# Kernel optimization log

Hardware: AMD Instinct MI355X
Metric: run time of the kernel (lower is better)

Reference implementation:

```python
import jax, jax.numpy as jnp
import numpy as np

BSZ, QLEN, KLEN = 2, 1024, 2048
QD = KD = VD = HID = 1024
NH = 16
HD = HID // NH
SCALE = 1.0 / (HD ** 0.5)
NEG_INF = -1e30


def setup_inputs() -> dict:
    key = jax.random.key(0)
    ks = jax.random.split(key, 8)
    query = jax.random.normal(ks[0], (BSZ, QLEN, QD), dtype=jnp.float32)
    k_in = jax.random.normal(ks[1], (BSZ, KLEN, KD), dtype=jnp.float32)
    v_in = jax.random.normal(ks[2], (BSZ, KLEN, VD), dtype=jnp.float32)
    attn_mask = jax.random.randint(ks[3], (BSZ, KLEN), 0, 2, dtype=jnp.int32)
    # xavier_uniform for Linear(in, out) without bias; stored as [in, out]
    def xavier(k, fan_in, fan_out):
        lim = (6.0 / (fan_in + fan_out)) ** 0.5
        return jax.random.uniform(k, (fan_in, fan_out), jnp.float32, -lim, lim)
    Wq = xavier(ks[4], QD, HID)
    Wk = xavier(ks[5], KD, HID)
    Wv = xavier(ks[6], VD, HID)
    Wo = xavier(ks[7], HID, QD)
    return {"query": query, "key": k_in, "value": v_in, "attn_mask": attn_mask,
            "Wq": Wq, "Wk": Wk, "Wv": Wv, "Wo": Wo}


def reference(query, key, value, attn_mask, Wq, Wk, Wv, Wo):
    bsz, qlen, _ = query.shape
    klen = key.shape[1]
    # projections -> [b, len, n_head, head_dim]
    head_q = (query @ Wq).reshape(bsz, qlen, NH, HD)
    head_k = (key @ Wk).reshape(bsz, klen, NH, HD)
    head_v = (value @ Wv).reshape(bsz, klen, NH, HD)
    # attn scores [b, i, j, n]
    attn_score = jnp.einsum('bind,bjnd->bijn', head_q, head_k) * SCALE
    # 2D mask [b, j]: broadcast over query dim (axis 1) and head dim (axis 3)
    mask = (attn_mask == 0)[:, None, :, None]
    attn_score = jnp.where(mask, NEG_INF, attn_score)
    # configurable activation: sigmoid (no normalization over klen)
    attn_prob = jax.nn.sigmoid(attn_score)
    attn_vec = jnp.einsum('bijn,bjnd->bind', attn_prob, head_v)
    attn_vec = attn_vec.reshape(bsz, qlen, HID)
    return attn_vec @ Wo
```

## Files before the change

### kernel.cpp

```cpp
#include <hip/hip_runtime.h>
#include <hip/hip_bf16.h>

#define BSZ 2
#define QLEN 1024
#define KLEN 2048
#define HID 1024
#define NH 16
#define HD 64
#define SCALE 0.125f

using f32x4 = __attribute__((ext_vector_type(4))) float;
using bf16x8 = __attribute__((ext_vector_type(8))) short;
using u32x4 = __attribute__((ext_vector_type(4))) unsigned int;
using u32x2 = __attribute__((ext_vector_type(2))) unsigned int;
typedef unsigned short u16;

__device__ __forceinline__ unsigned int cvtpk(float a, float b) {
    unsigned int r;
    asm("v_cvt_pk_bf16_f32 %0, %1, %2" : "=v"(r) : "v"(a), "v"(b));
    return r;
}
__device__ __forceinline__ unsigned int pack2bf(float a, float b) { return cvtpk(a, b); }
__device__ __forceinline__ u16 f2bf(float x) { return (u16)cvtpk(x, x); }
__device__ __forceinline__ f32x4 zero4() {
    f32x4 z = {0.0f, 0.0f, 0.0f, 0.0f};
    return z;
}

__device__ __forceinline__ void gl16(const void* g, void* l) {
    __builtin_amdgcn_global_load_lds(
        (const __attribute__((address_space(1))) void*)g,
        (__attribute__((address_space(3))) void*)l, 16, 0, 0);
}

template<int ROWS>
__device__ __forceinline__ void stage64(const u16* __restrict__ g, size_t gstride,
                                        u16* lds, int tid) {
    const int lane = tid & 63, wv = tid >> 6;
    constexpr int RPW = ROWS / 4;
#pragma unroll
    for (int c = 0; c < RPW / 8; ++c) {
        int row = wv * RPW + c * 8 + (lane >> 3);
        int cg = (lane & 7) ^ (row & 7);
        gl16(g + (size_t)row * gstride + cg * 8, lds + (size_t)(wv * RPW + c * 8) * 64);
    }
}

__global__ __launch_bounds__(256) void a2bf_kernel(
    const float* __restrict__ Aq, const float* __restrict__ Ak,
    const float* __restrict__ Av,
    u16* __restrict__ qbf, u16* __restrict__ kbf, u16* __restrict__ vbf)
{
    const int bid = blockIdx.x;
    const float* src; u16* dst; size_t base;
    if (bid < 1024)      { src = Aq; dst = qbf; base = (size_t)bid * 2048; }
    else if (bid < 3072) { src = Ak; dst = kbf; base = (size_t)(bid - 1024) * 2048; }
    else                 { src = Av; dst = vbf; base = (size_t)(bid - 3072) * 2048; }
    size_t e = base + (size_t)threadIdx.x * 8;
    float4 x0 = *(const float4*)&src[e];
    float4 x1 = *(const float4*)&src[e + 4];
    u32x4 w;
    w[0] = pack2bf(x0.x, x0.y); w[1] = pack2bf(x0.z, x0.w);
    w[2] = pack2bf(x1.x, x1.y); w[3] = pack2bf(x1.z, x1.w);
    *(u32x4*)&dst[e] = w;
}

__global__ __launch_bounds__(256) void wtrans_kernel(
    const float* __restrict__ W0, const float* __restrict__ W1,
    const float* __restrict__ W2, const float* __restrict__ W3,
    u16* __restrict__ T0, u16* __restrict__ T1,
    u16* __restrict__ T2, u16* __restrict__ T3)
{
    const float* W = blockIdx.z == 0 ? W0 : blockIdx.z == 1 ? W1 : blockIdx.z == 2 ? W2 : W3;
    u16* T = blockIdx.z == 0 ? T0 : blockIdx.z == 1 ? T1 : blockIdx.z == 2 ? T2 : T3;
    __shared__ float tile[64][65];
    const int tid = threadIdx.x;
    const int r0 = blockIdx.x * 64;
    const int c0 = blockIdx.y * 64;
#pragma unroll
    for (int i = 0; i < 4; ++i) {
        int ch = i * 256 + tid;
        int row = ch >> 4, cg = ch & 15;
        float4 x = *(const float4*)&W[(size_t)(r0 + row) * 1024 + c0 + cg * 4];
        tile[row][cg * 4 + 0] = x.x;
        tile[row][cg * 4 + 1] = x.y;
        tile[row][cg * 4 + 2] = x.z;
        tile[row][cg * 4 + 3] = x.w;
    }
    __syncthreads();
#pragma unroll
    for (int i = 0; i < 2; ++i) {
        int ch = i * 256 + tid;
        int orow = ch >> 3, ocg = ch & 7;
        u32x4 o;
#pragma unroll
        for (int j = 0; j < 4; ++j)
            o[j] = pack2bf(tile[ocg * 8 + 2 * j][orow], tile[ocg * 8 + 2 * j + 1][orow]);
        *(u32x4*)&T[(size_t)(c0 + orow) * 1024 + r0 + ocg * 8] = o;
    }
}

__global__ __launch_bounds__(256) void qkv_gemm_kernel(
    const u16* __restrict__ Aq, const u16* __restrict__ Ak, const u16* __restrict__ Av,
    const u16* __restrict__ Bq, const u16* __restrict__ Bk, const u16* __restrict__ Bv,
    u16* __restrict__ hq, u16* __restrict__ hk, u16* __restrict__ hvT)
{
    __shared__ u32x4 lds[2048];
    u16* As = (u16*)lds;
    u16* Bs = (u16*)(lds + 1024);

    const int i = blockIdx.x;
    const int bid = (i & 7) * 80 + (i >> 3);
    const u16* A; const u16* Bt; u16* C; int lb, task;
    if (bid < 128)      { task = 0; A = Aq; Bt = Bq; C = hq; lb = bid; }
    else if (bid < 384) { task = 1; A = Ak; Bt = Bk; C = hk; lb = bid - 128; }
    else                { task = 2; A = Av; Bt = Bv; C = nullptr; lb = bid - 384; }
    const int m0 = (lb >> 3) * 128, n0 = (lb & 7) * 128;

    const int tid = threadIdx.x;
    const int lane = tid & 63, wv = tid >> 6;
    const int wr = wv >> 1, wc = wv & 1;
    const int m = lane & 15, g = lane >> 4;

    f32x4 acc[4][4];
#pragma unroll
    for (int i2 = 0; i2 < 4; ++i2)
#pragma unroll
        for (int j = 0; j < 4; ++j) acc[i2][j] = zero4();

    for (int k0 = 0; k0 < 1024; k0 += 64) {
        stage64<128>(A  + (size_t)m0 * 1024 + k0, 1024, As, tid);
        stage64<128>(Bt + (size_t)n0 * 1024 + k0, 1024, Bs, tid);
        __syncthreads();
#pragma unroll
        for (int kk = 0; kk < 64; kk += 32) {
            bf16x8 af[4], bfr[4];
#pragma unroll
            for (int mi = 0; mi < 4; ++mi) {
                int row = wr * 64 + mi * 16 + m;
                af[mi] = *(const bf16x8*)&As[(row * 64 + kk + g * 8) ^ ((row & 7) << 3)];
            }
#pragma unroll
            for (int ni = 0; ni < 4; ++ni) {
                int row = wc * 64 + ni * 16 + m;
                bfr[ni] = *(const bf16x8*)&Bs[(row * 64 + kk + g * 8) ^ ((row & 7) << 3)];
            }
#pragma unroll
            for (int mi = 0; mi < 4; ++mi)
#pragma unroll
                for (int ni = 0; ni < 4; ++ni)
                    acc[mi][ni] = __builtin_amdgcn_mfma_f32_16x16x32_bf16(
                        af[mi], bfr[ni], acc[mi][ni], 0, 0, 0);
        }
        __syncthreads();
    }

    if (task < 2) {
#pragma unroll
        for (int mi = 0; mi < 4; ++mi)
#pragma unroll
            for (int r = 0; r < 4; ++r) {
                int row = m0 + wr * 64 + mi * 16 + g * 4 + r;
#pragma unroll
                for (int ni = 0; ni < 4; ++ni) {
                    int col = n0 + wc * 64 + ni * 16 + m;
                    C[(size_t)row * HID + col] = f2bf(acc[mi][ni][r]);
                }
            }
    } else {
        u16* T = (u16*)lds;
        __syncthreads();
#pragma unroll
        for (int mi = 0; mi < 4; ++mi)
#pragma unroll
            for (int ni = 0; ni < 4; ++ni)
#pragma unroll
                for (int r = 0; r < 4; ++r) {
                    int row = wr * 64 + mi * 16 + g * 4 + r;
                    int col = wc * 64 + ni * 16 + m;
                    T[col * 128 + ((((row >> 3) ^ (col & 7)) << 3) + (row & 7))] =
                        f2bf(acc[mi][ni][r]);
                }
        __syncthreads();
        const int b = m0 >> 11, kv0 = m0 & 2047;
#pragma unroll
        for (int it = 0; it < 8; ++it) {
            int idx = it * 256 + tid;
            int orow = idx >> 4, og = idx & 15;
            u32x4 x = *(const u32x4*)&T[orow * 128 + ((og ^ (orow & 7)) << 3)];
            *(u32x4*)&hvT[(size_t)(b * HID + n0 + orow) * KLEN + kv0 + og * 8] = x;
        }
    }
}

__device__ __forceinline__ void attn_tile(
    const u16* __restrict__ Ks, const u16* __restrict__ Vt,
    const float* __restrict__ Mlc, u16* __restrict__ P,
    bf16x8 qf0, bf16x8 qf1, int m, int g, f32x4* o)
{
#pragma unroll
    for (int sub = 0; sub < 2; ++sub) {
#pragma unroll
        for (int t = 0; t < 2; ++t) {
            int kvr = sub * 32 + t * 16 + m;
            bf16x8 ak0 = *(const bf16x8*)&Ks[(kvr * 64 + g * 8) ^ ((kvr & 7) << 3)];
            bf16x8 ak1 = *(const bf16x8*)&Ks[(kvr * 64 + 32 + g * 8) ^ ((kvr & 7) << 3)];
            f32x4 s = zero4();
            s = __builtin_amdgcn_mfma_f32_16x16x32_bf16(ak0, qf0, s, 0, 0, 0);
            s = __builtin_amdgcn_mfma_f32_16x16x32_bf16(ak1, qf1, s, 0, 0, 0);
            f32x4 mk = *(const f32x4*)&Mlc[sub * 32 + t * 16 + 4 * g];
            float p0 = mk[0] * __builtin_amdgcn_rcpf(1.0f + __expf(s[0] * -SCALE));
            float p1 = mk[1] * __builtin_amdgcn_rcpf(1.0f + __expf(s[1] * -SCALE));
            float p2 = mk[2] * __builtin_amdgcn_rcpf(1.0f + __expf(s[2] * -SCALE));
            float p3 = mk[3] * __builtin_amdgcn_rcpf(1.0f + __expf(s[3] * -SCALE));
            u32x2 pp = { cvtpk(p0, p1), cvtpk(p2, p3) };
            *(u32x2*)&P[m * 40 + t * 16 + 4 * g] = pp;
        }
        bf16x8 pa = *(const bf16x8*)&P[m * 40 + 8 * g];
#pragma unroll
        for (int nt = 0; nt < 4; ++nt) {
            int d = 16 * nt + m;
            bf16x8 vt = *(const bf16x8*)&Vt[(d * 64 + sub * 32 + g * 8) ^ ((d & 7) << 3)];
            o[nt] = __builtin_amdgcn_mfma_f32_16x16x32_bf16(pa, vt, o[nt], 0, 0, 0);
        }
    }
}

__global__ __launch_bounds__(256) void attn_kernel(
    const u16* __restrict__ hq, const u16* __restrict__ hk,
    const u16* __restrict__ hvT, const int* __restrict__ amask,
    float* __restrict__ O0, float* __restrict__ O1)
{
    __shared__ u32x4 KsBuf[2][512];
    __shared__ u32x4 VtBuf[2][512];
    __shared__ __align__(16) float Ml[2][64];
    __shared__ __align__(16) u16 Pw[4][16 * 40];

    const int tid = threadIdx.x;
    const int lane = tid & 63, wv = tid >> 6;
    const int m = lane & 15, g = lane >> 4;
    const int li = blockIdx.x;
    const int bid = (li & 7) * 128 + (li >> 3);
    const int qt = bid & 15, h = (bid >> 4) & 15, z = bid >> 8;
    const int b = z >> 1, sp = z & 1;
    const int qrow0 = qt * 64 + wv * 16;
    float* Op = sp ? O1 : O0;
    u16* P = Pw[wv];
    u16* Ks0 = (u16*)KsBuf[0]; u16* Ks1 = (u16*)KsBuf[1];
    u16* Vt0 = (u16*)VtBuf[0]; u16* Vt1 = (u16*)VtBuf[1];

    const u16* qp = &hq[(size_t)(b * QLEN + qrow0 + m) * HID + h * HD + g * 8];
    bf16x8 qf0 = *(const bf16x8*)qp;
    bf16x8 qf1 = *(const bf16x8*)(qp + 32);

    const u16* kbase = hk + (size_t)(b * KLEN + sp * 1024) * HID + h * HD;
    const u16* vbase = hvT + (size_t)(b * HID + h * HD) * KLEN + sp * 1024;
    const int* mbase = amask + b * KLEN + sp * 1024;

    f32x4 o[4];
#pragma unroll
    for (int i = 0; i < 4; ++i) o[i] = zero4();

    stage64<64>(kbase, HID, Ks0, tid);
    stage64<64>(vbase, KLEN, Vt0, tid);
    if (tid < 64) Ml[0][tid] = (mbase[tid] != 0) ? 1.0f : 0.0f;
    __syncthreads();

#pragma unroll 1
    for (int it = 0; it < 16; it += 2) {
        stage64<64>(kbase + (size_t)(it + 1) * 64 * HID, HID, Ks1, tid);
        stage64<64>(vbase + (it + 1) * 64, KLEN, Vt1, tid);
        if (tid < 64) Ml[1][tid] = (mbase[(it + 1) * 64 + tid] != 0) ? 1.0f : 0.0f;
        attn_tile(Ks0, Vt0, Ml[0], P, qf0, qf1, m, g, o);
        __syncthreads();
        if (it + 2 < 16) {
            stage64<64>(kbase + (size_t)(it + 2) * 64 * HID, HID, Ks0, tid);
            stage64<64>(vbase + (it + 2) * 64, KLEN, Vt0, tid);
            if (tid < 64) Ml[0][tid] = (mbase[(it + 2) * 64 + tid] != 0) ? 1.0f : 0.0f;
        }
        attn_tile(Ks1, Vt1, Ml[1], P, qf0, qf1, m, g, o);
        __syncthreads();
    }
#pragma unroll
    for (int nt = 0; nt < 4; ++nt)
#pragma unroll
        for (int r = 0; r < 4; ++r)
            Op[(size_t)(b * QLEN + qrow0 + 4 * g + r) * HID + h * HD + 16 * nt + m] =
                o[nt][r];
}

__global__ __launch_bounds__(256) void oproj_kernel(
    const float* __restrict__ O0, const float* __restrict__ O1,
    const u16* __restrict__ Bt, float* __restrict__ out)
{
    __shared__ u32x4 lds[1536];
    u16* As = (u16*)lds;
    u16* Bs = (u16*)(lds + 512);

    const int tid = threadIdx.x;
    const int lane = tid & 63, wv = tid >> 6;
    const int wr = wv >> 1, wc = wv & 1;
    const int m = lane & 15, g = lane >> 4;
    const int m0 = blockIdx.x * 64, n0 = blockIdx.y * 128;

    f32x4 acc[2][4];
#pragma unroll
    for (int i = 0; i < 2; ++i)
#pragma unroll
        for (int j = 0; j < 4; ++j) acc[i][j] = zero4();

    for (int k0 = 0; k0 < 1024; k0 += 64) {
        stage64<128>(Bt + (size_t)n0 * 1024 + k0, 1024, Bs, tid);
#pragma unroll
        for (int c = 0; c < 2; ++c) {
            int idx = c * 256 + tid;
            int row = idx >> 3, cg = idx & 7;
            size_t off = (size_t)(m0 + row) * 1024 + k0 + cg * 8;
            float4 a0 = *(const float4*)&O0[off];
            float4 a1 = *(const float4*)&O0[off + 4];
            float4 b0 = *(const float4*)&O1[off];
            float4 b1 = *(const float4*)&O1[off + 4];
            u32x4 w;
            w[0] = pack2bf(a0.x + b0.x, a0.y + b0.y);
            w[1] = pack2bf(a0.z + b0.z, a0.w + b0.w);
            w[2] = pack2bf(a1.x + b1.x, a1.y + b1.y);
            w[3] = pack2bf(a1.z + b1.z, a1.w + b1.w);
            *(u32x4*)&As[(row * 64 + cg * 8) ^ ((row & 7) << 3)] = w;
        }
        __syncthreads();
#pragma unroll
        for (int kk = 0; kk < 64; kk += 32) {
            bf16x8 af[2], bfr[4];
#pragma unroll
            for (int mi = 0; mi < 2; ++mi) {
                int row = wr * 32 + mi * 16 + m;
                af[mi] = *(const bf16x8*)&As[(row * 64 + kk + g * 8) ^ ((row & 7) << 3)];
            }
#pragma unroll
            for (int ni = 0; ni < 4; ++ni) {
                int row = wc * 64 + ni * 16 + m;
                bfr[ni] = *(const bf16x8*)&Bs[(row * 64 + kk + g * 8) ^ ((row & 7) << 3)];
            }
#pragma unroll
            for (int mi = 0; mi < 2; ++mi)
#pragma unroll
                for (int ni = 0; ni < 4; ++ni)
                    acc[mi][ni] = __builtin_amdgcn_mfma_f32_16x16x32_bf16(
                        af[mi], bfr[ni], acc[mi][ni], 0, 0, 0);
        }
        __syncthreads();
    }
#pragma unroll
    for (int mi = 0; mi < 2; ++mi)
#pragma unroll
        for (int r = 0; r < 4; ++r) {
            int row = m0 + wr * 32 + mi * 16 + g * 4 + r;
#pragma unroll
            for (int ni = 0; ni < 4; ++ni) {
                int col = n0 + wc * 64 + ni * 16 + m;
                out[(size_t)row * HID + col] = acc[mi][ni][r];
            }
        }
}

extern "C" void kernel_launch(void* const* d_in, const int* in_sizes, int n_in,
                              void* d_out, int out_size, void* d_ws, size_t ws_size,
                              hipStream_t stream)
{
    const float* query = (const float*)d_in[0];
    const float* key   = (const float*)d_in[1];
    const float* value = (const float*)d_in[2];
    const int*   amask = (const int*)d_in[3];
    const float* Wq    = (const float*)d_in[4];
    const float* Wk    = (const float*)d_in[5];
    const float* Wv    = (const float*)d_in[6];
    const float* Wo    = (const float*)d_in[7];

    char* ws = (char*)d_ws;
    u16* wtq = (u16*)(ws + (0ull  << 20));
    u16* wtk = (u16*)(ws + (2ull  << 20));
    u16* wtv = (u16*)(ws + (4ull  << 20));
    u16* wto = (u16*)(ws + (6ull  << 20));
    u16* hq  = (u16*)(ws + (8ull  << 20));
    u16* hk  = (u16*)(ws + (12ull << 20));
    u16* hvT = (u16*)(ws + (20ull << 20));
    u16* qbf = (u16*)(ws + (28ull << 20));
    u16* kbf = (u16*)(ws + (32ull << 20));
    u16* vbf = (u16*)(ws + (40ull << 20));
    float* O0 = (float*)(ws + (28ull << 20));
    float* O1 = (float*)(ws + (36ull << 20));

    a2bf_kernel<<<dim3(5120), 256, 0, stream>>>(query, key, value, qbf, kbf, vbf);
    wtrans_kernel<<<dim3(16, 16, 4), 256, 0, stream>>>(Wq, Wk, Wv, Wo, wtq, wtk, wtv, wto);
    qkv_gemm_kernel<<<dim3(640), 256, 0, stream>>>(qbf, kbf, vbf, wtq, wtk, wtv, hq, hk, hvT);
    attn_kernel<<<dim3(1024), 256, 0, stream>>>(hq, hk, hvT, amask, O0, O1);
    oproj_kernel<<<dim3(32, 8), 256, 0, stream>>>(O0, O1, wto, (float*)d_out);
}
```

Measured before the change: 202.0 us.

## Double-buffer GEMMs, drop attention KV split, emit bf16 attention output, merge prep kernels

QKV and output-projection GEMMs switch to two LDS buffers so the next k-slice loads while the current one is multiplied. The attention kernel no longer splits keys into two halves with fp32 partial outputs. It loops over all keys and writes a single bf16 result, so the output projection stages it directly with async loads instead of summing two fp32 arrays. The activation-conversion and weight-transpose kernels are merged into one launch. This halves the attention grid, which may reduce occupancy and tail balance.

```diff
diff --git a/kernel.cpp b/kernel.cpp
--- a/kernel.cpp
+++ b/kernel.cpp
@@ -46,37 +46,38 @@
     }
 }
 
-__global__ __launch_bounds__(256) void a2bf_kernel(
+__global__ __launch_bounds__(256) void prep_kernel(
     const float* __restrict__ Aq, const float* __restrict__ Ak,
     const float* __restrict__ Av,
-    u16* __restrict__ qbf, u16* __restrict__ kbf, u16* __restrict__ vbf)
-{
-    const int bid = blockIdx.x;
-    const float* src; u16* dst; size_t base;
-    if (bid < 1024)      { src = Aq; dst = qbf; base = (size_t)bid * 2048; }
-    else if (bid < 3072) { src = Ak; dst = kbf; base = (size_t)(bid - 1024) * 2048; }
-    else                 { src = Av; dst = vbf; base = (size_t)(bid - 3072) * 2048; }
-    size_t e = base + (size_t)threadIdx.x * 8;
-    float4 x0 = *(const float4*)&src[e];
-    float4 x1 = *(const float4*)&src[e + 4];
-    u32x4 w;
-    w[0] = pack2bf(x0.x, x0.y); w[1] = pack2bf(x0.z, x0.w);
-    w[2] = pack2bf(x1.x, x1.y); w[3] = pack2bf(x1.z, x1.w);
-    *(u32x4*)&dst[e] = w;
-}
-
-__global__ __launch_bounds__(256) void wtrans_kernel(
     const float* __restrict__ W0, const float* __restrict__ W1,
     const float* __restrict__ W2, const float* __restrict__ W3,
+    u16* __restrict__ qbf, u16* __restrict__ kbf, u16* __restrict__ vbf,
     u16* __restrict__ T0, u16* __restrict__ T1,
     u16* __restrict__ T2, u16* __restrict__ T3)
 {
-    const float* W = blockIdx.z == 0 ? W0 : blockIdx.z == 1 ? W1 : blockIdx.z == 2 ? W2 : W3;
-    u16* T = blockIdx.z == 0 ? T0 : blockIdx.z == 1 ? T1 : blockIdx.z == 2 ? T2 : T3;
     __shared__ float tile[64][65];
+    const int bid = blockIdx.x;
     const int tid = threadIdx.x;
-    const int r0 = blockIdx.x * 64;
-    const int c0 = blockIdx.y * 64;
+    if (bid < 5120) {
+        const float* src; u16* dst; size_t base;
+        if (bid < 1024)      { src = Aq; dst = qbf; base = (size_t)bid * 2048; }
+        else if (bid < 3072) { src = Ak; dst = kbf; base = (size_t)(bid - 1024) * 2048; }
+        else                 { src = Av; dst = vbf; base = (size_t)(bid - 3072) * 2048; }
+        size_t e = base + (size_t)tid * 8;
+        float4 x0 = *(const float4*)&src[e];
+        float4 x1 = *(const float4*)&src[e + 4];
+        u32x4 w;
+        w[0] = pack2bf(x0.x, x0.y); w[1] = pack2bf(x0.z, x0.w);
+        w[2] = pack2bf(x1.x, x1.y); w[3] = pack2bf(x1.z, x1.w);
+        *(u32x4*)&dst[e] = w;
+        return;
+    }
+    const int lb = bid - 5120;
+    const int zi = lb >> 8;
+    const float* W = zi == 0 ? W0 : zi == 1 ? W1 : zi == 2 ? W2 : W3;
+    u16* T = zi == 0 ? T0 : zi == 1 ? T1 : zi == 2 ? T2 : T3;
+    const int r0 = (lb & 15) * 64;
+    const int c0 = ((lb >> 4) & 15) * 64;
 #pragma unroll
     for (int i = 0; i < 4; ++i) {
         int ch = i * 256 + tid;
@@ -100,14 +101,42 @@
     }
 }
 
+__device__ __forceinline__ void gemm_step128(
+    const u16* __restrict__ As, const u16* __restrict__ Bs,
+    int wr, int wc, int m, int g, f32x4 (*acc)[4])
+{
+#pragma unroll
+    for (int kk = 0; kk < 64; kk += 32) {
+        bf16x8 af[4], bfr[4];
+#pragma unroll
+        for (int mi = 0; mi < 4; ++mi) {
+            int row = wr * 64 + mi * 16 + m;
+            af[mi] = *(const bf16x8*)&As[(row * 64 + kk + g * 8) ^ ((row & 7) << 3)];
+        }
+#pragma unroll
+        for (int ni = 0; ni < 4; ++ni) {
+            int row = wc * 64 + ni * 16 + m;
+            bfr[ni] = *(const bf16x8*)&Bs[(row * 64 + kk + g * 8) ^ ((row & 7) << 3)];
+        }
+#pragma unroll
+        for (int mi = 0; mi < 4; ++mi)
+#pragma unroll
+            for (int ni = 0; ni < 4; ++ni)
+                acc[mi][ni] = __builtin_amdgcn_mfma_f32_16x16x32_bf16(
+                    af[mi], bfr[ni], acc[mi][ni], 0, 0, 0);
+    }
+}
+
 __global__ __launch_bounds__(256) void qkv_gemm_kernel(
     const u16* __restrict__ Aq, const u16* __restrict__ Ak, const u16* __restrict__ Av,
     const u16* __restrict__ Bq, const u16* __restrict__ Bk, const u16* __restrict__ Bv,
     u16* __restrict__ hq, u16* __restrict__ hk, u16* __restrict__ hvT)
 {
-    __shared__ u32x4 lds[2048];
-    u16* As = (u16*)lds;
-    u16* Bs = (u16*)(lds + 1024);
+    __shared__ u32x4 lds[4096];
+    u16* As0 = (u16*)lds;
+    u16* Bs0 = (u16*)(lds + 1024);
+    u16* As1 = (u16*)(lds + 2048);
+    u16* Bs1 = (u16*)(lds + 3072);
 
     const int i = blockIdx.x;
     const int bid = (i & 7) * 80 + (i >> 3);
@@ -122,36 +151,29 @@
     const int wr = wv >> 1, wc = wv & 1;
     const int m = lane & 15, g = lane >> 4;
 
+    const u16* Ab = A  + (size_t)m0 * 1024;
+    const u16* Bb = Bt + (size_t)n0 * 1024;
+
     f32x4 acc[4][4];
 #pragma unroll
     for (int i2 = 0; i2 < 4; ++i2)
 #pragma unroll
         for (int j = 0; j < 4; ++j) acc[i2][j] = zero4();
 
-    for (int k0 = 0; k0 < 1024; k0 += 64) {
-        stage64<128>(A  + (size_t)m0 * 1024 + k0, 1024, As, tid);
-        stage64<128>(Bt + (size_t)n0 * 1024 + k0, 1024, Bs, tid);
-        __syncthreads();
-#pragma unroll
-        for (int kk = 0; kk < 64; kk += 32) {
-            bf16x8 af[4], bfr[4];
-#pragma unroll
-            for (int mi = 0; mi < 4; ++mi) {
-                int row = wr * 64 + mi * 16 + m;
-                af[mi] = *(const bf16x8*)&As[(row * 64 + kk + g * 8) ^ ((row & 7) << 3)];
-            }
-#pragma unroll
-            for (int ni = 0; ni < 4; ++ni) {
-                int row = wc * 64 + ni * 16 + m;
-                bfr[ni] = *(const bf16x8*)&Bs[(row * 64 + kk + g * 8) ^ ((row & 7) << 3)];
-            }
-#pragma unroll
-            for (int mi = 0; mi < 4; ++mi)
-#pragma unroll
-                for (int ni = 0; ni < 4; ++ni)
-                    acc[mi][ni] = __builtin_amdgcn_mfma_f32_16x16x32_bf16(
-                        af[mi], bfr[ni], acc[mi][ni], 0, 0, 0);
-        }
+    stage64<128>(Ab, 1024, As0, tid);
+    stage64<128>(Bb, 1024, Bs0, tid);
+    __syncthreads();
+#pragma unroll 1
+    for (int k0 = 0; k0 < 1024; k0 += 128) {
+        stage64<128>(Ab + k0 + 64, 1024, As1, tid);
+        stage64<128>(Bb + k0 + 64, 1024, Bs1, tid);
+        gemm_step128(As0, Bs0, wr, wc, m, g, acc);
+        __syncthreads();
+        if (k0 + 128 < 1024) {
+            stage64<128>(Ab + k0 + 128, 1024, As0, tid);
+            stage64<128>(Bb + k0 + 128, 1024, Bs0, tid);
+        }
+        gemm_step128(As1, Bs1, wr, wc, m, g, acc);
         __syncthreads();
     }
 
@@ -169,7 +191,6 @@
             }
     } else {
         u16* T = (u16*)lds;
-        __syncthreads();
 #pragma unroll
         for (int mi = 0; mi < 4; ++mi)
 #pragma unroll
@@ -229,7 +250,7 @@
 __global__ __launch_bounds__(256) void attn_kernel(
     const u16* __restrict__ hq, const u16* __restrict__ hk,
     const u16* __restrict__ hvT, const int* __restrict__ amask,
-    float* __restrict__ O0, float* __restrict__ O1)
+    u16* __restrict__ av)
 {
     __shared__ u32x4 KsBuf[2][512];
     __shared__ u32x4 VtBuf[2][512];
@@ -240,11 +261,9 @@
     const int lane = tid & 63, wv = tid >> 6;
     const int m = lane & 15, g = lane >> 4;
     const int li = blockIdx.x;
-    const int bid = (li & 7) * 128 + (li >> 3);
-    const int qt = bid & 15, h = (bid >> 4) & 15, z = bid >> 8;
-    const int b = z >> 1, sp = z & 1;
+    const int bid = (li & 7) * 64 + (li >> 3);
+    const int qt = bid & 15, h = (bid >> 4) & 15, b = bid >> 8;
     const int qrow0 = qt * 64 + wv * 16;
-    float* Op = sp ? O1 : O0;
     u16* P = Pw[wv];
     u16* Ks0 = (u16*)KsBuf[0]; u16* Ks1 = (u16*)KsBuf[1];
     u16* Vt0 = (u16*)VtBuf[0]; u16* Vt1 = (u16*)VtBuf[1];
@@ -253,9 +272,9 @@
     bf16x8 qf0 = *(const bf16x8*)qp;
     bf16x8 qf1 = *(const bf16x8*)(qp + 32);
 
-    const u16* kbase = hk + (size_t)(b * KLEN + sp * 1024) * HID + h * HD;
-    const u16* vbase = hvT + (size_t)(b * HID + h * HD) * KLEN + sp * 1024;
-    const int* mbase = amask + b * KLEN + sp * 1024;
+    const u16* kbase = hk + (size_t)(b * KLEN) * HID + h * HD;
+    const u16* vbase = hvT + (size_t)(b * HID + h * HD) * KLEN;
+    const int* mbase = amask + b * KLEN;
 
     f32x4 o[4];
 #pragma unroll
@@ -267,13 +286,13 @@
     __syncthreads();
 
 #pragma unroll 1
-    for (int it = 0; it < 16; it += 2) {
+    for (int it = 0; it < 32; it += 2) {
         stage64<64>(kbase + (size_t)(it + 1) * 64 * HID, HID, Ks1, tid);
         stage64<64>(vbase + (it + 1) * 64, KLEN, Vt1, tid);
         if (tid < 64) Ml[1][tid] = (mbase[(it + 1) * 64 + tid] != 0) ? 1.0f : 0.0f;
         attn_tile(Ks0, Vt0, Ml[0], P, qf0, qf1, m, g, o);
         __syncthreads();
-        if (it + 2 < 16) {
+        if (it + 2 < 32) {
             stage64<64>(kbase + (size_t)(it + 2) * 64 * HID, HID, Ks0, tid);
             stage64<64>(vbase + (it + 2) * 64, KLEN, Vt0, tid);
             if (tid < 64) Ml[0][tid] = (mbase[(it + 2) * 64 + tid] != 0) ? 1.0f : 0.0f;
@@ -285,23 +304,55 @@
     for (int nt = 0; nt < 4; ++nt)
 #pragma unroll
         for (int r = 0; r < 4; ++r)
-            Op[(size_t)(b * QLEN + qrow0 + 4 * g + r) * HID + h * HD + 16 * nt + m] =
-                o[nt][r];
+            av[(size_t)(b * QLEN + qrow0 + 4 * g + r) * HID + h * HD + 16 * nt + m] =
+                f2bf(o[nt][r]);
+}
+
+__device__ __forceinline__ void oproj_step(
+    const u16* __restrict__ As, const u16* __restrict__ Bs,
+    int wr, int wc, int m, int g, f32x4 (*acc)[4])
+{
+#pragma unroll
+    for (int kk = 0; kk < 64; kk += 32) {
+        bf16x8 af[2], bfr[4];
+#pragma unroll
+        for (int mi = 0; mi < 2; ++mi) {
+            int row = wr * 32 + mi * 16 + m;
+            af[mi] = *(const bf16x8*)&As[(row * 64 + kk + g * 8) ^ ((row & 7) << 3)];
+        }
+#pragma unroll
+        for (int ni = 0; ni < 4; ++ni) {
+            int row = wc * 64 + ni * 16 + m;
+            bfr[ni] = *(const bf16x8*)&Bs[(row * 64 + kk + g * 8) ^ ((row & 7) << 3)];
+        }
+#pragma unroll
+        for (int mi = 0; mi < 2; ++mi)
+#pragma unroll
+            for (int ni = 0; ni < 4; ++ni)
+                acc[mi][ni] = __builtin_amdgcn_mfma_f32_16x16x32_bf16(
+                    af[mi], bfr[ni], acc[mi][ni], 0, 0, 0);
+    }
 }
 
 __global__ __launch_bounds__(256) void oproj_kernel(
-    const float* __restrict__ O0, const float* __restrict__ O1,
-    const u16* __restrict__ Bt, float* __restrict__ out)
-{
-    __shared__ u32x4 lds[1536];
-    u16* As = (u16*)lds;
-    u16* Bs = (u16*)(lds + 512);
+    const u16* __restrict__ av, const u16* __restrict__ Bt, float* __restrict__ out)
+{
+    __shared__ u32x4 lds[3072];
+    u16* As0 = (u16*)lds;
+    u16* Bs0 = (u16*)(lds + 512);
+    u16* As1 = (u16*)(lds + 1536);
+    u16* Bs1 = (u16*)(lds + 2048);
 
     const int tid = threadIdx.x;
     const int lane = tid & 63, wv = tid >> 6;
     const int wr = wv >> 1, wc = wv & 1;
     const int m = lane & 15, g = lane >> 4;
-    const int m0 = blockIdx.x * 64, n0 = blockIdx.y * 128;
+    const int li = blockIdx.x;
+    const int bid = (li & 7) * 32 + (li >> 3);
+    const int m0 = (bid & 31) * 64, n0 = (bid >> 5) * 128;
+
+    const u16* Ab = av + (size_t)m0 * 1024;
+    const u16* Bb = Bt + (size_t)n0 * 1024;
 
     f32x4 acc[2][4];
 #pragma unroll
@@ -309,45 +360,20 @@
 #pragma unroll
         for (int j = 0; j < 4; ++j) acc[i][j] = zero4();
 
-    for (int k0 = 0; k0 < 1024; k0 += 64) {
-        stage64<128>(Bt + (size_t)n0 * 1024 + k0, 1024, Bs, tid);
-#pragma unroll
-        for (int c = 0; c < 2; ++c) {
-            int idx = c * 256 + tid;
-            int row = idx >> 3, cg = idx & 7;
-            size_t off = (size_t)(m0 + row) * 1024 + k0 + cg * 8;
-            float4 a0 = *(const float4*)&O0[off];
-            float4 a1 = *(const float4*)&O0[off + 4];
-            float4 b0 = *(const float4*)&O1[off];
-            float4 b1 = *(const float4*)&O1[off + 4];
-            u32x4 w;
-            w[0] = pack2bf(a0.x + b0.x, a0.y + b0.y);
-            w[1] = pack2bf(a0.z + b0.z, a0.w + b0.w);
-            w[2] = pack2bf(a1.x + b1.x, a1.y + b1.y);
-            w[3] = pack2bf(a1.z + b1.z, a1.w + b1.w);
-            *(u32x4*)&As[(row * 64 + cg * 8) ^ ((row & 7) << 3)] = w;
-        }
-        __syncthreads();
-#pragma unroll
-        for (int kk = 0; kk < 64; kk += 32) {
-            bf16x8 af[2], bfr[4];
-#pragma unroll
-            for (int mi = 0; mi < 2; ++mi) {
-                int row = wr * 32 + mi * 16 + m;
-                af[mi] = *(const bf16x8*)&As[(row * 64 + kk + g * 8) ^ ((row & 7) << 3)];
-            }
-#pragma unroll
-            for (int ni = 0; ni < 4; ++ni) {
-                int row = wc * 64 + ni * 16 + m;
-                bfr[ni] = *(const bf16x8*)&Bs[(row * 64 + kk + g * 8) ^ ((row & 7) << 3)];
-            }
-#pragma unroll
-            for (int mi = 0; mi < 2; ++mi)
-#pragma unroll
-                for (int ni = 0; ni < 4; ++ni)
-                    acc[mi][ni] = __builtin_amdgcn_mfma_f32_16x16x32_bf16(
-                        af[mi], bfr[ni], acc[mi][ni], 0, 0, 0);
-        }
+    stage64<64>(Ab, 1024, As0, tid);
+    stage64<128>(Bb, 1024, Bs0, tid);
+    __syncthreads();
+#pragma unroll 1
+    for (int k0 = 0; k0 < 1024; k0 += 128) {
+        stage64<64>(Ab + k0 + 64, 1024, As1, tid);
+        stage64<128>(Bb + k0 + 64, 1024, Bs1, tid);
+        oproj_step(As0, Bs0, wr, wc, m, g, acc);
+        __syncthreads();
+        if (k0 + 128 < 1024) {
+            stage64<64>(Ab + k0 + 128, 1024, As0, tid);
+            stage64<128>(Bb + k0 + 128, 1024, Bs0, tid);
+        }
+        oproj_step(As1, Bs1, wr, wc, m, g, acc);
         __syncthreads();
     }
 #pragma unroll
@@ -387,12 +413,11 @@
     u16* qbf = (u16*)(ws + (28ull << 20));
     u16* kbf = (u16*)(ws + (32ull << 20));
     u16* vbf = (u16*)(ws + (40ull << 20));
-    float* O0 = (float*)(ws + (28ull << 20));
-    float* O1 = (float*)(ws + (36ull << 20));
-
-    a2bf_kernel<<<dim3(5120), 256, 0, stream>>>(query, key, value, qbf, kbf, vbf);
-    wtrans_kernel<<<dim3(16, 16, 4), 256, 0, stream>>>(Wq, Wk, Wv, Wo, wtq, wtk, wtv, wto);
+    u16* av  = (u16*)(ws + (28ull << 20));
+
+    prep_kernel<<<dim3(6144), 256, 0, stream>>>(query, key, value, Wq, Wk, Wv, Wo,
+                                                qbf, kbf, vbf, wtq, wtk, wtv, wto);
     qkv_gemm_kernel<<<dim3(640), 256, 0, stream>>>(qbf, kbf, vbf, wtq, wtk, wtv, hq, hk, hvT);
-    attn_kernel<<<dim3(1024), 256, 0, stream>>>(hq, hk, hvT, amask, O0, O1);
-    oproj_kernel<<<dim3(32, 8), 256, 0, stream>>>(O0, O1, wto, (float*)d_out);
-}
+    attn_kernel<<<dim3(512), 256, 0, stream>>>(hq, hk, hvT, amask, av);
+    oproj_kernel<<<dim3(256), 256, 0, stream>>>(av, wto, (float*)d_out);
+}
```

New measurement: 190.4 us. 1.06x faster.

## Merge prep kernels and double-buffer LDS in QKV projection GEMM

Applied to the files above, without the earlier changes.

Merges the activation bf16 conversion and the weight transpose into one prep kernel launch, which removes a launch and its inter-kernel gap. The QKV GEMM now uses two LDS buffers, so the async global-to-LDS loads for the next K slice overlap the MFMA work on the current one, and it needs one barrier per slice instead of two. This doubles the LDS footprint per block to 64KB, which may lower occupancy.

```diff
diff --git a/kernel.cpp b/kernel.cpp
--- a/kernel.cpp
+++ b/kernel.cpp
@@ -46,37 +46,38 @@
     }
 }
 
-__global__ __launch_bounds__(256) void a2bf_kernel(
+__global__ __launch_bounds__(256) void prep_kernel(
     const float* __restrict__ Aq, const float* __restrict__ Ak,
     const float* __restrict__ Av,
-    u16* __restrict__ qbf, u16* __restrict__ kbf, u16* __restrict__ vbf)
-{
-    const int bid = blockIdx.x;
-    const float* src; u16* dst; size_t base;
-    if (bid < 1024)      { src = Aq; dst = qbf; base = (size_t)bid * 2048; }
-    else if (bid < 3072) { src = Ak; dst = kbf; base = (size_t)(bid - 1024) * 2048; }
-    else                 { src = Av; dst = vbf; base = (size_t)(bid - 3072) * 2048; }
-    size_t e = base + (size_t)threadIdx.x * 8;
-    float4 x0 = *(const float4*)&src[e];
-    float4 x1 = *(const float4*)&src[e + 4];
-    u32x4 w;
-    w[0] = pack2bf(x0.x, x0.y); w[1] = pack2bf(x0.z, x0.w);
-    w[2] = pack2bf(x1.x, x1.y); w[3] = pack2bf(x1.z, x1.w);
-    *(u32x4*)&dst[e] = w;
-}
-
-__global__ __launch_bounds__(256) void wtrans_kernel(
     const float* __restrict__ W0, const float* __restrict__ W1,
     const float* __restrict__ W2, const float* __restrict__ W3,
+    u16* __restrict__ qbf, u16* __restrict__ kbf, u16* __restrict__ vbf,
     u16* __restrict__ T0, u16* __restrict__ T1,
     u16* __restrict__ T2, u16* __restrict__ T3)
 {
-    const float* W = blockIdx.z == 0 ? W0 : blockIdx.z == 1 ? W1 : blockIdx.z == 2 ? W2 : W3;
-    u16* T = blockIdx.z == 0 ? T0 : blockIdx.z == 1 ? T1 : blockIdx.z == 2 ? T2 : T3;
     __shared__ float tile[64][65];
+    const int bid = blockIdx.x;
     const int tid = threadIdx.x;
-    const int r0 = blockIdx.x * 64;
-    const int c0 = blockIdx.y * 64;
+    if (bid < 5120) {
+        const float* src; u16* dst; size_t base;
+        if (bid < 1024)      { src = Aq; dst = qbf; base = (size_t)bid * 2048; }
+        else if (bid < 3072) { src = Ak; dst = kbf; base = (size_t)(bid - 1024) * 2048; }
+        else                 { src = Av; dst = vbf; base = (size_t)(bid - 3072) * 2048; }
+        size_t e = base + (size_t)tid * 8;
+        float4 x0 = *(const float4*)&src[e];
+        float4 x1 = *(const float4*)&src[e + 4];
+        u32x4 w;
+        w[0] = pack2bf(x0.x, x0.y); w[1] = pack2bf(x0.z, x0.w);
+        w[2] = pack2bf(x1.x, x1.y); w[3] = pack2bf(x1.z, x1.w);
+        *(u32x4*)&dst[e] = w;
+        return;
+    }
+    const int lb = bid - 5120;
+    const int zi = lb >> 8;
+    const float* W = zi == 0 ? W0 : zi == 1 ? W1 : zi == 2 ? W2 : W3;
+    u16* T = zi == 0 ? T0 : zi == 1 ? T1 : zi == 2 ? T2 : T3;
+    const int r0 = (lb & 15) * 64;
+    const int c0 = ((lb >> 4) & 15) * 64;
 #pragma unroll
     for (int i = 0; i < 4; ++i) {
         int ch = i * 256 + tid;
@@ -100,14 +101,42 @@
     }
 }
 
+__device__ __forceinline__ void gemm_step128(
+    const u16* __restrict__ As, const u16* __restrict__ Bs,
+    int wr, int wc, int m, int g, f32x4 (*acc)[4])
+{
+#pragma unroll
+    for (int kk = 0; kk < 64; kk += 32) {
+        bf16x8 af[4], bfr[4];
+#pragma unroll
+        for (int mi = 0; mi < 4; ++mi) {
+            int row = wr * 64 + mi * 16 + m;
+            af[mi] = *(const bf16x8*)&As[(row * 64 + kk + g * 8) ^ ((row & 7) << 3)];
+        }
+#pragma unroll
+        for (int ni = 0; ni < 4; ++ni) {
+            int row = wc * 64 + ni * 16 + m;
+            bfr[ni] = *(const bf16x8*)&Bs[(row * 64 + kk + g * 8) ^ ((row & 7) << 3)];
+        }
+#pragma unroll
+        for (int mi = 0; mi < 4; ++mi)
+#pragma unroll
+            for (int ni = 0; ni < 4; ++ni)
+                acc[mi][ni] = __builtin_amdgcn_mfma_f32_16x16x32_bf16(
+                    af[mi], bfr[ni], acc[mi][ni], 0, 0, 0);
+    }
+}
+
 __global__ __launch_bounds__(256) void qkv_gemm_kernel(
     const u16* __restrict__ Aq, const u16* __restrict__ Ak, const u16* __restrict__ Av,
     const u16* __restrict__ Bq, const u16* __restrict__ Bk, const u16* __restrict__ Bv,
     u16* __restrict__ hq, u16* __restrict__ hk, u16* __restrict__ hvT)
 {
-    __shared__ u32x4 lds[2048];
-    u16* As = (u16*)lds;
-    u16* Bs = (u16*)(lds + 1024);
+    __shared__ u32x4 lds[4096];
+    u16* As0 = (u16*)lds;
+    u16* Bs0 = (u16*)(lds + 1024);
+    u16* As1 = (u16*)(lds + 2048);
+    u16* Bs1 = (u16*)(lds + 3072);
 
     const int i = blockIdx.x;
     const int bid = (i & 7) * 80 + (i >> 3);
@@ -122,36 +151,29 @@
     const int wr = wv >> 1, wc = wv & 1;
     const int m = lane & 15, g = lane >> 4;
 
+    const u16* Ab = A  + (size_t)m0 * 1024;
+    const u16* Bb = Bt + (size_t)n0 * 1024;
+
     f32x4 acc[4][4];
 #pragma unroll
     for (int i2 = 0; i2 < 4; ++i2)
 #pragma unroll
         for (int j = 0; j < 4; ++j) acc[i2][j] = zero4();
 
-    for (int k0 = 0; k0 < 1024; k0 += 64) {
-        stage64<128>(A  + (size_t)m0 * 1024 + k0, 1024, As, tid);
-        stage64<128>(Bt + (size_t)n0 * 1024 + k0, 1024, Bs, tid);
-        __syncthreads();
-#pragma unroll
-        for (int kk = 0; kk < 64; kk += 32) {
-            bf16x8 af[4], bfr[4];
-#pragma unroll
-            for (int mi = 0; mi < 4; ++mi) {
-                int row = wr * 64 + mi * 16 + m;
-                af[mi] = *(const bf16x8*)&As[(row * 64 + kk + g * 8) ^ ((row & 7) << 3)];
-            }
-#pragma unroll
-            for (int ni = 0; ni < 4; ++ni) {
-                int row = wc * 64 + ni * 16 + m;
-                bfr[ni] = *(const bf16x8*)&Bs[(row * 64 + kk + g * 8) ^ ((row & 7) << 3)];
-            }
-#pragma unroll
-            for (int mi = 0; mi < 4; ++mi)
-#pragma unroll
-                for (int ni = 0; ni < 4; ++ni)
-                    acc[mi][ni] = __builtin_amdgcn_mfma_f32_16x16x32_bf16(
-                        af[mi], bfr[ni], acc[mi][ni], 0, 0, 0);
-        }
+    stage64<128>(Ab, 1024, As0, tid);
+    stage64<128>(Bb, 1024, Bs0, tid);
+    __syncthreads();
+#pragma unroll 1
+    for (int k0 = 0; k0 < 1024; k0 += 128) {
+        stage64<128>(Ab + k0 + 64, 1024, As1, tid);
+        stage64<128>(Bb + k0 + 64, 1024, Bs1, tid);
+        gemm_step128(As0, Bs0, wr, wc, m, g, acc);
+        __syncthreads();
+        if (k0 + 128 < 1024) {
+            stage64<128>(Ab + k0 + 128, 1024, As0, tid);
+            stage64<128>(Bb + k0 + 128, 1024, Bs0, tid);
+        }
+        gemm_step128(As1, Bs1, wr, wc, m, g, acc);
         __syncthreads();
     }
 
@@ -169,7 +191,6 @@
             }
     } else {
         u16* T = (u16*)lds;
-        __syncthreads();
 #pragma unroll
         for (int mi = 0; mi < 4; ++mi)
 #pragma unroll
@@ -390,9 +411,10 @@
     float* O0 = (float*)(ws + (28ull << 20));
     float* O1 = (float*)(ws + (36ull << 20));
 
-    a2bf_kernel<<<dim3(5120), 256, 0, stream>>>(query, key, value, qbf, kbf, vbf);
-    wtrans_kernel<<<dim3(16, 16, 4), 256, 0, stream>>>(Wq, Wk, Wv, Wo, wtq, wtk, wtv, wto);
-    qkv_gemm_kernel<<<dim3(640), 256, 0, stream>>>(qbf, kbf, vbf, wtq, wtk, wtv, hq, hk, hvT);
+    prep_kernel<<<dim3(6144), 256, 0, stream>>>(query, key, value, Wq, Wk, Wv, Wo,
+                                                qbf, kbf, vbf, wtq, wtk, wtv, wto);
+    qkv_gemm_kernel<<<dim3(640), 256, 0, stream>>>(qbf, kbf, vbf, wtq, wtk, wtv,
+                                                   hq, hk, hvT);
     attn_kernel<<<dim3(1024), 256, 0, stream>>>(hq, hk, hvT, amask, O0, O1);
     oproj_kernel<<<dim3(32, 8), 256, 0, stream>>>(O0, O1, wto, (float*)d_out);
 }
```

Measured after the change: 189.6 us. 6.2% less time.
